# Optimization experiments

Measured on AMD Instinct MI355X. Metric: run time of the kernel, lower is better.

## Reference

```python
import jax, jax.numpy as jnp
import numpy as np

B, T, D, K, H = 32, 500, 128, 64, 8  # batch, target_dim, input_size, lin_hidden, num_att_heads
NEG = -9e15


def _xavier(k, shape):
    fan_in, fan_out = shape[-2], shape[-1]
    lim = float(np.sqrt(6.0 / (fan_in + fan_out)))
    return jax.random.uniform(k, shape, jnp.float32, -lim, lim)


def setup_inputs() -> dict:
    key = jax.random.key(0)
    ks = jax.random.split(key, 20)
    return {
        "inputs": jax.random.normal(ks[0], (B, T, D), jnp.float32),
        "hidden": jax.random.normal(ks[1], (B, T, K), jnp.float32),
        "linear": _xavier(ks[2], (H, D, K)),
        "bias": jnp.zeros((1, K), jnp.float32),
        "att_src": _xavier(ks[3], (H, K, 1)),
        "att_tar": _xavier(ks[4], (H, K, 1)),
        "W_hr": _xavier(ks[5], (K, K)),
        "W_hi": _xavier(ks[6], (K, K)),
        "W_hm": _xavier(ks[7], (K, K)),
        "W_ir": _xavier(ks[8], (D, K)), "b_ir": jnp.zeros((K,), jnp.float32),
        "W_ii": _xavier(ks[9], (D, K)), "b_ii": jnp.zeros((K,), jnp.float32),
        "W_in": _xavier(ks[10], (D, K)), "b_in": jnp.zeros((K,), jnp.float32),
        "mlp_W1": _xavier(ks[11], (K, K)), "mlp_b1": jnp.zeros((K,), jnp.float32),
        "mlp_W2": _xavier(ks[12], (K, K)), "mlp_b2": jnp.zeros((K,), jnp.float32),
        "proj_W": _xavier(ks[13], (K * T, 2 * T)), "proj_b": jnp.zeros((2 * T,), jnp.float32),
    }


def reference(inputs, hidden, linear, bias, att_src, att_tar,
              W_hr, W_hi, W_hm, W_ir, b_ir, W_ii, b_ii, W_in, b_in,
              mlp_W1, mlp_b1, mlp_W2, mlp_b2, proj_W, proj_b):
    # per-head projection: [H, B, T, K]  (att_hidden == 0 -> h_att is h)
    h = jnp.einsum('btd,hdk->hbtk', inputs, linear)
    h_src = jnp.einsum('hbtk,hko->hbto', h, att_src)  # [H,B,T,1]
    h_tar = jnp.einsum('hbtk,hko->hbto', h, att_tar)  # [H,B,T,1]
    # additive attention score via broadcast: [H,B,T,T]
    score = jax.nn.leaky_relu(h_tar + jnp.swapaxes(h_src, -1, -2), 0.2)
    adj_mask = ~jnp.eye(T, dtype=bool)  # adj = ones - eye
    score = jnp.where(adj_mask, score, NEG)
    att = jax.nn.softmax(score, axis=-1)
    msgs = jnp.einsum('hbts,hbsk->hbtk', att, h).mean(axis=0)  # mean over heads -> [B,T,K]
    msgs = jnp.tanh(msgs + bias)
    # GRU-style gated update
    inp_r = inputs @ W_ir + b_ir
    inp_i = inputs @ W_ii + b_ii
    inp_n = inputs @ W_in + b_in
    m = jax.nn.sigmoid(inp_r + msgs @ W_hr)
    i = jax.nn.sigmoid(inp_i + msgs @ W_hi)
    n = jnp.tanh(inp_n + m * (msgs @ W_hm))
    hidden_new = i * n + (1.0 - i) * hidden
    # out MLP (Linear-ReLU-Linear)
    pred = jax.nn.relu(hidden_new @ mlp_W1 + mlp_b1) @ mlp_W2 + mlp_b2
    # distribution-args projection on flattened features: loc, softplus(scale)
    dargs = pred.reshape(pred.shape[0], -1) @ proj_W + proj_b  # [B, 2T]
    loc, scale_raw = dargs[:, :T], dargs[:, T:]
    scale = jax.nn.softplus(scale_raw)
    return (loc, scale, hidden_new)
```

## Files before the change

kernel.cpp:

```cpp
#include <hip/hip_runtime.h>
#include <hip/hip_bf16.h>
#include <math.h>


#define BB 32
#define TT 500
#define DD 128
#define KK 64
#define HH 8

typedef short bf16x8 __attribute__((ext_vector_type(8)));
typedef float f32x16 __attribute__((ext_vector_type(16)));

static __device__ __forceinline__ unsigned short f2bf(float x) {
    __hip_bfloat16 h = __float2bfloat16(x);
    return *reinterpret_cast<unsigned short*>(&h);
}

__global__ __launch_bounds__(256) void k1_h(
        const float* __restrict__ inputs, const float* __restrict__ linear,
        const float* __restrict__ att_src, const float* __restrict__ att_tar,
        unsigned short* __restrict__ hT, float* __restrict__ src_ws,
        float* __restrict__ tar_ws) {
    __shared__ __align__(16) float lin_s[DD * KK];
    __shared__ __align__(16) float inp_s[64 * DD];
    __shared__ float asrc_s[KK], atar_s[KK];
    const int t0 = blockIdx.x * 64;
    const int b  = blockIdx.y;
    const int hh = blockIdx.z;
    const int tid = threadIdx.x;
    const int k = tid & 63, tq = tid >> 6;

    for (int e = tid; e < DD * KK; e += 256) lin_s[e] = linear[hh * DD * KK + e];
    for (int e = tid; e < 64 * DD; e += 256) {
        int row = e >> 7, d = e & 127;
        int t = t0 + row;
        inp_s[e] = (t < TT) ? inputs[(b * TT + t) * DD + d] : 0.f;
    }
    if (tid < KK) { asrc_s[tid] = att_src[hh * KK + tid]; atar_s[tid] = att_tar[hh * KK + tid]; }
    __syncthreads();

    float acc[16];
#pragma unroll
    for (int i = 0; i < 16; ++i) acc[i] = 0.f;

    for (int d4 = 0; d4 < DD / 4; ++d4) {
        float l0 = lin_s[(d4 * 4 + 0) * KK + k];
        float l1 = lin_s[(d4 * 4 + 1) * KK + k];
        float l2 = lin_s[(d4 * 4 + 2) * KK + k];
        float l3 = lin_s[(d4 * 4 + 3) * KK + k];
#pragma unroll
        for (int i = 0; i < 16; ++i) {
            const float4 iv = *(const float4*)&inp_s[(tq * 16 + i) * DD + d4 * 4];
            acc[i] += iv.x * l0 + iv.y * l1 + iv.z * l2 + iv.w * l3;
        }
    }
    const long hb = (long)hh * BB + b;
    {
        union { unsigned short u[16]; int4 v[2]; } pk;
#pragma unroll
        for (int i = 0; i < 16; ++i) pk.u[i] = f2bf(acc[i]);
        unsigned short* hp = hT + hb * (64L * 512) + (long)k * 512 + t0 + tq * 16;
        *(int4*)(hp)     = pk.v[0];
        *(int4*)(hp + 8) = pk.v[1];
    }
    const float sv = asrc_s[k], tv = atar_s[k];
#pragma unroll
    for (int i = 0; i < 16; ++i) {
        float ss = acc[i] * sv, ts = acc[i] * tv;
#pragma unroll
        for (int o = 32; o > 0; o >>= 1) { ss += __shfl_xor(ss, o); ts += __shfl_xor(ts, o); }
        int t = t0 + tq * 16 + i;
        if (k == 0 && t < TT) { src_ws[hb * TT + t] = ss; tar_ws[hb * TT + t] = ts; }
    }
}

__global__ __launch_bounds__(256) void k2_attn(
        const unsigned short* __restrict__ hT, const float* __restrict__ src_ws,
        const float* __restrict__ tar_ws, float* __restrict__ msgs) {
    __shared__ float srcv[512];
    __shared__ float red[4];
    __shared__ float partial[4][64];
    __shared__ float drow[64];
    __shared__ __align__(16) unsigned short es[64 * 128];
    __shared__ __align__(16) unsigned short hs[64 * 128];

    const int t0 = blockIdx.x * 64;
    const int b  = blockIdx.y;
    const int hh = blockIdx.z;
    const int tid = threadIdx.x;
    const long hb = (long)hh * BB + b;
    const float* srcp = src_ws + hb * TT;

    for (int e = tid; e < 512; e += 256) srcv[e] = (e < TT) ? srcp[e] : -3.0e38f;
    __syncthreads();
    float sm = -3.0e38f;
    for (int e = tid; e < 512; e += 256) sm = fmaxf(sm, srcv[e]);
#pragma unroll
    for (int o = 32; o > 0; o >>= 1) sm = fmaxf(sm, __shfl_xor(sm, o));
    if ((tid & 63) == 0) red[tid >> 6] = sm;
    __syncthreads();
    const float Smax = fmaxf(fmaxf(red[0], red[1]), fmaxf(red[2], red[3]));

    const int tl = tid & 63, g = tid >> 6;
    const int tglob = t0 + tl;
    const float tv = (tglob < TT) ? tar_ws[hb * TT + tglob] : 0.f;
    const float xm = tv + Smax;
    const float ml = fmaxf(xm, 0.2f * xm);

    const unsigned short* hTg = hT + hb * (64L * 512);
    const int lane = tid & 63, wid = tid >> 6;
    const int wr = wid >> 1, wc = wid & 1;
    f32x16 acc;
#pragma unroll
    for (int r = 0; r < 16; ++r) acc[r] = 0.f;

    float lsum = 0.f;
    for (int s0 = 0; s0 < 512; s0 += 128) {
#pragma unroll
        for (int p = 0; p < 4; ++p) {
            const int r = p * 16 + (tid >> 4), c = tid & 15;
            const int4 hv = *(const int4*)(hTg + (long)r * 512 + s0 + c * 8);
            const int wa = (r * 256 + c * 16) ^ ((r & 7) << 4);
            *(int4*)((char*)hs + wa) = hv;
        }
#pragma unroll
        for (int i = 0; i < 4; ++i) {
            const int sl = g * 8 + i * 32;
            const int sg = s0 + sl;
            union { unsigned short u[8]; int4 v; } pk;
#pragma unroll
            for (int j = 0; j < 8; ++j) {
                float x = tv + srcv[sg + j];
                float l = fmaxf(x, 0.2f * x);
                float e = __expf(l - ml);
                if (sg + j == tglob) e = 0.f;
                lsum += e;
                pk.u[j] = f2bf(e);
            }
            const int wa = (tl * 256 + sl * 2) ^ ((tl & 7) << 4);
            *(int4*)((char*)es + wa) = pk.v;
        }
        __syncthreads();
#pragma unroll
        for (int st = 0; st < 8; ++st) {
            const int sA = st * 16 + (lane >> 5) * 8;
            const int arow = wr * 32 + (lane & 31);
            const int brow = wc * 32 + (lane & 31);
            bf16x8 av = *(bf16x8*)((char*)es + ((arow * 256 + sA * 2) ^ ((arow & 7) << 4)));
            bf16x8 bv = *(bf16x8*)((char*)hs + ((brow * 256 + sA * 2) ^ ((brow & 7) << 4)));
            acc = __builtin_amdgcn_mfma_f32_32x32x16_bf16(av, bv, acc, 0, 0, 0);
        }
        __syncthreads();
    }
    partial[g][tl] = lsum;
    __syncthreads();
    if (tid < 64) {
        float s = partial[0][tid] + partial[1][tid] + partial[2][tid] + partial[3][tid];
        drow[tid] = 1.f / s;
    }
    __syncthreads();
#pragma unroll
    for (int r = 0; r < 16; ++r) {
        const int row = wr * 32 + (r & 3) + 8 * (r >> 2) + 4 * (lane >> 5);
        const int t = t0 + row;
        if (t < TT) {
            const float v = acc[r] * drow[row] * 0.125f;
            atomicAdd(&msgs[((long)b * TT + t) * KK + (wc * 32 + (lane & 31))], v);
        }
    }
}

__global__ __launch_bounds__(256) void k3_gru(
        const float* __restrict__ inputs, const float* __restrict__ hidden,
        const float* __restrict__ bias,
        const float* __restrict__ W_hr, const float* __restrict__ W_hi, const float* __restrict__ W_hm,
        const float* __restrict__ W_ir, const float* __restrict__ b_ir,
        const float* __restrict__ W_ii, const float* __restrict__ b_ii,
        const float* __restrict__ W_in, const float* __restrict__ b_in,
        const float* __restrict__ W1, const float* __restrict__ b1,
        const float* __restrict__ W2, const float* __restrict__ b2,
        const float* __restrict__ msgs, float* __restrict__ out_hidden,
        float* __restrict__ pred) {
    const int tid = threadIdx.x;
    const int lane = tid & 63, w = tid >> 6;
    const int row = blockIdx.x * 4 + w;
    const float* inp = inputs + (long)row * DD;

    float mg = tanhf(msgs[(long)row * KK + lane] + bias[lane]);
    float hr = 0.f, hi = 0.f, hm = 0.f;
#pragma unroll 8
    for (int j = 0; j < KK; ++j) {
        float v = __shfl(mg, j);
        hr += v * W_hr[j * KK + lane];
        hi += v * W_hi[j * KK + lane];
        hm += v * W_hm[j * KK + lane];
    }
    float i0 = inp[lane], i1 = inp[64 + lane];
    float ir = 0.f, ii = 0.f, inn = 0.f;
#pragma unroll 8
    for (int j = 0; j < 64; ++j) {
        float v = __shfl(i0, j);
        ir  += v * W_ir[j * KK + lane];
        ii  += v * W_ii[j * KK + lane];
        inn += v * W_in[j * KK + lane];
    }
#pragma unroll 8
    for (int j = 0; j < 64; ++j) {
        float v = __shfl(i1, j);
        ir  += v * W_ir[(64 + j) * KK + lane];
        ii  += v * W_ii[(64 + j) * KK + lane];
        inn += v * W_in[(64 + j) * KK + lane];
    }
    float m  = 1.f / (1.f + expf(-(ir + b_ir[lane] + hr)));
    float ig = 1.f / (1.f + expf(-(ii + b_ii[lane] + hi)));
    float n  = tanhf(inn + b_in[lane] + m * hm);
    float hnew = ig * n + (1.f - ig) * hidden[(long)row * KK + lane];
    out_hidden[(long)row * KK + lane] = hnew;

    float a1 = 0.f;
#pragma unroll 8
    for (int j = 0; j < KK; ++j) a1 += __shfl(hnew, j) * W1[j * KK + lane];
    a1 = fmaxf(a1 + b1[lane], 0.f);
    float pr = 0.f;
#pragma unroll 8
    for (int j = 0; j < KK; ++j) pr += __shfl(a1, j) * W2[j * KK + lane];
    pred[(long)row * KK + lane] = pr + b2[lane];
}

__global__ __launch_bounds__(256) void k3b_transpose(
        const float* __restrict__ pred, float* __restrict__ predT) {
    __shared__ float Tl[64][36];
    const int r0 = blockIdx.x * 64;
    const int tid = threadIdx.x;
    {
        const int b = tid >> 3, q = tid & 7;
        const float* pb = pred + (long)b * 32000 + r0;
#pragma unroll
        for (int j = 0; j < 2; ++j) {
            const int r = q * 8 + j * 4;
            const float4 v = *(const float4*)&pb[r];
            Tl[r + 0][b] = v.x; Tl[r + 1][b] = v.y;
            Tl[r + 2][b] = v.z; Tl[r + 3][b] = v.w;
        }
    }
    __syncthreads();
    {
        const int r = tid >> 2, bq = tid & 3;
        float* op = predT + (long)(r0 + r) * 32 + bq * 8;
        *(float4*)(op)     = *(const float4*)&Tl[r][bq * 8];
        *(float4*)(op + 4) = *(const float4*)&Tl[r][bq * 8 + 4];
    }
}

#define FMA4(A, S, W) { (A).x += (S)*(W).x; (A).y += (S)*(W).y; (A).z += (S)*(W).z; (A).w += (S)*(W).w; }
__global__ __launch_bounds__(256) void k4_proj(
        const float* __restrict__ predT, const float* __restrict__ proj_W,
        float* __restrict__ part) {
    __shared__ float red[3][4096];
    const int tid = threadIdx.x;
    const int lane = tid & 63, w = tid >> 6;
    const int c = blockIdx.x * 256 + lane * 4;
    const bool cok = (c < 1000);
    const int r0w = blockIdx.y * 256 + w * 64;
    const int r0s = __builtin_amdgcn_readfirstlane(r0w);
    const float* pw = predT + (long)r0s * 32;
    const float* wp = proj_W + (long)r0w * 1000 + c;

    float4 acc[32];
#pragma unroll
    for (int b = 0; b < 32; ++b) acc[b] = float4{0.f, 0.f, 0.f, 0.f};

    const float4 f4z = {0.f, 0.f, 0.f, 0.f};
    float4 wbuf[4];
#pragma unroll
    for (int i = 0; i < 4; ++i)
        wbuf[i] = cok ? *(const float4*)&wp[(long)i * 1000] : f4z;

    for (int ch = 0; ch < 16; ++ch) {
#pragma unroll
        for (int i = 0; i < 4; ++i) {
            const int r = ch * 4 + i;
            const float4 wv = wbuf[i];
            const int rn = r + 4;
            if (rn < 64) wbuf[i] = cok ? *(const float4*)&wp[(long)rn * 1000] : f4z;
            const float* pr = pw + r * 32;
#pragma unroll
            for (int b4 = 0; b4 < 8; ++b4) {
                const float4 p4 = *(const float4*)&pr[b4 * 4];
                FMA4(acc[b4 * 4 + 0], p4.x, wv);
                FMA4(acc[b4 * 4 + 1], p4.y, wv);
                FMA4(acc[b4 * 4 + 2], p4.z, wv);
                FMA4(acc[b4 * 4 + 3], p4.w, wv);
            }
        }
    }
#pragma unroll
    for (int half = 0; half < 2; ++half) {
        const int bs = half * 16;
        if (w > 0) {
#pragma unroll
            for (int b = 0; b < 16; ++b) {
                red[w - 1][(b * 4 + 0) * 64 + lane] = acc[bs + b].x;
                red[w - 1][(b * 4 + 1) * 64 + lane] = acc[bs + b].y;
                red[w - 1][(b * 4 + 2) * 64 + lane] = acc[bs + b].z;
                red[w - 1][(b * 4 + 3) * 64 + lane] = acc[bs + b].w;
            }
        }
        __syncthreads();
        if (w == 0) {
#pragma unroll
            for (int b = 0; b < 16; ++b) {
                acc[bs + b].x += red[0][(b*4+0)*64+lane] + red[1][(b*4+0)*64+lane] + red[2][(b*4+0)*64+lane];
                acc[bs + b].y += red[0][(b*4+1)*64+lane] + red[1][(b*4+1)*64+lane] + red[2][(b*4+1)*64+lane];
                acc[bs + b].z += red[0][(b*4+2)*64+lane] + red[1][(b*4+2)*64+lane] + red[2][(b*4+2)*64+lane];
                acc[bs + b].w += red[0][(b*4+3)*64+lane] + red[1][(b*4+3)*64+lane] + red[2][(b*4+3)*64+lane];
            }
        }
        __syncthreads();
    }
    if (w == 0 && cok) {
#pragma unroll
        for (int b = 0; b < 32; ++b)
            *(float4*)&part[((long)blockIdx.y * 32 + b) * 1000 + c] = acc[b];
    }
}

__global__ __launch_bounds__(256) void k5_final(
        const float* __restrict__ part, const float* __restrict__ proj_b,
        float* __restrict__ out) {
    const int idx = blockIdx.x * 256 + threadIdx.x;
    float v = 0.f;
    for (int y = 0; y < 125; ++y) v += part[(long)y * 32000 + idx];
    const int b = idx / 1000, cc = idx % 1000;
    v += proj_b[cc];
    if (cc < TT) {
        out[b * TT + cc] = v;
    } else {
        float sp = fmaxf(v, 0.f) + log1pf(expf(-fabsf(v)));
        out[BB * TT + b * TT + (cc - TT)] = sp;
    }
}

extern "C" void kernel_launch(void* const* d_in, const int* in_sizes, int n_in,
                              void* d_out, int out_size, void* d_ws, size_t ws_size,
                              hipStream_t stream) {
    const float* inputs  = (const float*)d_in[0];
    const float* hidden  = (const float*)d_in[1];
    const float* linear  = (const float*)d_in[2];
    const float* bias    = (const float*)d_in[3];
    const float* att_src = (const float*)d_in[4];
    const float* att_tar = (const float*)d_in[5];
    const float* W_hr = (const float*)d_in[6];
    const float* W_hi = (const float*)d_in[7];
    const float* W_hm = (const float*)d_in[8];
    const float* W_ir = (const float*)d_in[9];
    const float* b_ir = (const float*)d_in[10];
    const float* W_ii = (const float*)d_in[11];
    const float* b_ii = (const float*)d_in[12];
    const float* W_in = (const float*)d_in[13];
    const float* b_in = (const float*)d_in[14];
    const float* W1 = (const float*)d_in[15];
    const float* b1 = (const float*)d_in[16];
    const float* W2 = (const float*)d_in[17];
    const float* b2 = (const float*)d_in[18];
    const float* proj_W = (const float*)d_in[19];
    const float* proj_b = (const float*)d_in[20];

    unsigned short* hT = (unsigned short*)d_ws;
    float* part = (float*)d_ws;
    float* fbase  = (float*)(hT + 8388608);
    float* src_ws = fbase;
    float* tar_ws = src_ws + (size_t)HH * BB * TT;
    float* msgs   = tar_ws + (size_t)HH * BB * TT;
    float* pred   = msgs + (size_t)BB * TT * KK;
    float* predT  = pred + (size_t)BB * TT * KK;

    float* out = (float*)d_out;
    float* out_hidden = out + 2 * BB * TT;

    hipMemsetAsync(msgs, 0, (size_t)BB * TT * KK * sizeof(float), stream);

    k1_h<<<dim3(8, BB, HH), 256, 0, stream>>>(inputs, linear, att_src, att_tar,
                                              hT, src_ws, tar_ws);
    k2_attn<<<dim3(8, BB, HH), 256, 0, stream>>>(hT, src_ws, tar_ws, msgs);
    k3_gru<<<4000, 256, 0, stream>>>(inputs, hidden, bias, W_hr, W_hi, W_hm,
                                     W_ir, b_ir, W_ii, b_ii, W_in, b_in,
                                     W1, b1, W2, b2, msgs, out_hidden, pred);
    k3b_transpose<<<500, 256, 0, stream>>>(pred, predT);
    k4_proj<<<dim3(4, 125), 256, 0, stream>>>(predT, proj_W, part);
    k5_final<<<125, 256, 0, stream>>>(part, proj_b, out);
}
```

Before: 501.4 us.

## Compute per-head projection with bf16 MFMA and pre-transposed weights

Replaces the scalar FP32 FMA loop in the head-projection kernel with 32x32x16 bf16 MFMA instructions. A new small kernel transposes the linear weights into bf16 once per call, and inputs are converted to bf16 into XOR-swizzled shared memory. The attention src/tar dot products are now reduced through shared memory across waves. This lowers compute and LDS traffic in the first stage, at the cost of bf16 rounding of the inputs and weights before the matmul and one extra launch.

```diff
diff --git a/kernel.cpp b/kernel.cpp
--- a/kernel.cpp
+++ b/kernel.cpp
@@ -17,61 +17,99 @@
     return *reinterpret_cast<unsigned short*>(&h);
 }
 
+__global__ __launch_bounds__(256) void k0_linT(
+        const float* __restrict__ linear, unsigned short* __restrict__ linT) {
+    const int h  = blockIdx.x >> 3;
+    const int kb = (blockIdx.x & 7) * 8;
+    const int kk = threadIdx.x >> 5;
+    const int d0 = (threadIdx.x & 31) * 4;
+    const float* lp = linear + (long)h * 8192 + (long)d0 * 64 + (kb + kk);
+    union { unsigned short u[4]; int2 v; } o;
+#pragma unroll
+    for (int j = 0; j < 4; ++j) o.u[j] = f2bf(lp[(long)j * 64]);
+    *(int2*)&linT[(long)h * 8192 + (kb + kk) * 128 + d0] = o.v;
+}
+
 __global__ __launch_bounds__(256) void k1_h(
-        const float* __restrict__ inputs, const float* __restrict__ linear,
+        const float* __restrict__ inputs, const unsigned short* __restrict__ linT,
         const float* __restrict__ att_src, const float* __restrict__ att_tar,
         unsigned short* __restrict__ hT, float* __restrict__ src_ws,
         float* __restrict__ tar_ws) {
-    __shared__ __align__(16) float lin_s[DD * KK];
-    __shared__ __align__(16) float inp_s[64 * DD];
+    __shared__ __align__(16) unsigned short inp_s[64 * 128];
+    __shared__ __align__(16) unsigned short lin_s[64 * 128];
     __shared__ float asrc_s[KK], atar_s[KK];
+    __shared__ float sred[2][64], tred[2][64];
     const int t0 = blockIdx.x * 64;
     const int b  = blockIdx.y;
     const int hh = blockIdx.z;
     const int tid = threadIdx.x;
-    const int k = tid & 63, tq = tid >> 6;
-
-    for (int e = tid; e < DD * KK; e += 256) lin_s[e] = linear[hh * DD * KK + e];
-    for (int e = tid; e < 64 * DD; e += 256) {
-        int row = e >> 7, d = e & 127;
-        int t = t0 + row;
-        inp_s[e] = (t < TT) ? inputs[(b * TT + t) * DD + d] : 0.f;
+    const int lane = tid & 63, wid = tid >> 6;
+    const int wr = wid >> 1, wc = wid & 1;
+    const long hb = (long)hh * BB + b;
+
+    {
+        const int r = tid >> 2, q = tid & 3;
+        const int t = t0 + r;
+        union { unsigned short u[8]; int4 v; } pk;
+#pragma unroll
+        for (int j = 0; j < 4; ++j) {
+            const int d0 = q * 32 + j * 8;
+            if (t < TT) {
+                const float4 a = *(const float4*)&inputs[((long)b * TT + t) * DD + d0];
+                const float4 c = *(const float4*)&inputs[((long)b * TT + t) * DD + d0 + 4];
+                pk.u[0] = f2bf(a.x); pk.u[1] = f2bf(a.y); pk.u[2] = f2bf(a.z); pk.u[3] = f2bf(a.w);
+                pk.u[4] = f2bf(c.x); pk.u[5] = f2bf(c.y); pk.u[6] = f2bf(c.z); pk.u[7] = f2bf(c.w);
+            } else {
+                pk.v = int4{0, 0, 0, 0};
+            }
+            *(int4*)((char*)inp_s + ((r * 256 + d0 * 2) ^ ((r & 7) << 4))) = pk.v;
+        }
+    }
+    {
+        const int r = tid >> 2, q = tid & 3;
+        const unsigned short* lp = linT + (long)hh * 8192 + r * 128 + q * 32;
+#pragma unroll
+        for (int j = 0; j < 4; ++j) {
+            const int d0 = q * 32 + j * 8;
+            *(int4*)((char*)lin_s + ((r * 256 + d0 * 2) ^ ((r & 7) << 4))) =
+                *(const int4*)(lp + j * 8);
+        }
     }
     if (tid < KK) { asrc_s[tid] = att_src[hh * KK + tid]; atar_s[tid] = att_tar[hh * KK + tid]; }
     __syncthreads();
 
-    float acc[16];
-#pragma unroll
-    for (int i = 0; i < 16; ++i) acc[i] = 0.f;
-
-    for (int d4 = 0; d4 < DD / 4; ++d4) {
-        float l0 = lin_s[(d4 * 4 + 0) * KK + k];
-        float l1 = lin_s[(d4 * 4 + 1) * KK + k];
-        float l2 = lin_s[(d4 * 4 + 2) * KK + k];
-        float l3 = lin_s[(d4 * 4 + 3) * KK + k];
-#pragma unroll
-        for (int i = 0; i < 16; ++i) {
-            const float4 iv = *(const float4*)&inp_s[(tq * 16 + i) * DD + d4 * 4];
-            acc[i] += iv.x * l0 + iv.y * l1 + iv.z * l2 + iv.w * l3;
-        }
-    }
-    const long hb = (long)hh * BB + b;
-    {
-        union { unsigned short u[16]; int4 v[2]; } pk;
-#pragma unroll
-        for (int i = 0; i < 16; ++i) pk.u[i] = f2bf(acc[i]);
-        unsigned short* hp = hT + hb * (64L * 512) + (long)k * 512 + t0 + tq * 16;
-        *(int4*)(hp)     = pk.v[0];
-        *(int4*)(hp + 8) = pk.v[1];
-    }
-    const float sv = asrc_s[k], tv = atar_s[k];
-#pragma unroll
-    for (int i = 0; i < 16; ++i) {
-        float ss = acc[i] * sv, ts = acc[i] * tv;
-#pragma unroll
-        for (int o = 32; o > 0; o >>= 1) { ss += __shfl_xor(ss, o); ts += __shfl_xor(ts, o); }
-        int t = t0 + tq * 16 + i;
-        if (k == 0 && t < TT) { src_ws[hb * TT + t] = ss; tar_ws[hb * TT + t] = ts; }
+    f32x16 acc;
+#pragma unroll
+    for (int r = 0; r < 16; ++r) acc[r] = 0.f;
+#pragma unroll
+    for (int st = 0; st < 8; ++st) {
+        const int sA = st * 16 + (lane >> 5) * 8;
+        const int arow = wr * 32 + (lane & 31);
+        const int brow = wc * 32 + (lane & 31);
+        bf16x8 av = *(bf16x8*)((char*)lin_s + ((arow * 256 + sA * 2) ^ ((arow & 7) << 4)));
+        bf16x8 bv = *(bf16x8*)((char*)inp_s + ((brow * 256 + sA * 2) ^ ((brow & 7) << 4)));
+        acc = __builtin_amdgcn_mfma_f32_32x32x16_bf16(av, bv, acc, 0, 0, 0);
+    }
+    float sp = 0.f, tp = 0.f;
+    unsigned short* hp = hT + hb * (64L * 512);
+    const int tcol = t0 + wc * 32 + (lane & 31);
+#pragma unroll
+    for (int r = 0; r < 16; ++r) {
+        const int kk = wr * 32 + (r & 3) + 8 * (r >> 2) + 4 * (lane >> 5);
+        hp[(long)kk * 512 + tcol] = f2bf(acc[r]);
+        sp += acc[r] * asrc_s[kk];
+        tp += acc[r] * atar_s[kk];
+    }
+    sp += __shfl_xor(sp, 32);
+    tp += __shfl_xor(tp, 32);
+    if (lane < 32) { sred[wr][wc * 32 + lane] = sp; tred[wr][wc * 32 + lane] = tp; }
+    __syncthreads();
+    if (tid < 64) {
+        const int t = t0 + tid;
+        if (t < TT) {
+            src_ws[hb * TT + t] = sred[0][tid] + sred[1][tid];
+            tar_ws[hb * TT + t] = tred[0][tid] + tred[1][tid];
+        }
     }
 }
 
@@ -375,13 +413,15 @@
     float* msgs   = tar_ws + (size_t)HH * BB * TT;
     float* pred   = msgs + (size_t)BB * TT * KK;
     float* predT  = pred + (size_t)BB * TT * KK;
+    unsigned short* linT = (unsigned short*)(predT + (size_t)BB * TT * KK);
 
     float* out = (float*)d_out;
     float* out_hidden = out + 2 * BB * TT;
 
     hipMemsetAsync(msgs, 0, (size_t)BB * TT * KK * sizeof(float), stream);
 
-    k1_h<<<dim3(8, BB, HH), 256, 0, stream>>>(inputs, linear, att_src, att_tar,
+    k0_linT<<<64, 256, 0, stream>>>(linear, linT);
+    k1_h<<<dim3(8, BB, HH), 256, 0, stream>>>(inputs, linT, att_src, att_tar,
                                               hT, src_ws, tar_ws);
     k2_attn<<<dim3(8, BB, HH), 256, 0, stream>>>(hT, src_ws, tar_ws, msgs);
     k3_gru<<<4000, 256, 0, stream>>>(inputs, hidden, bias, W_hr, W_hi, W_hm,
```

After: 419.9 us. -16.2%, faster.
